# Optimization experiments

Hardware: AMD Instinct MI355X
Metric: run time of the kernel (lower is better)

Reference implementation:

```python
import jax, jax.numpy as jnp
import numpy as np

TAU = 0.5
EPS = 1e-12  # F.normalize eps


def _l2_normalize(z):
    n = jnp.linalg.norm(z, axis=1, keepdims=True)
    return z / jnp.maximum(n, EPS)


def _semi_loss(a, b):
    # a, b: [N, d], already raw embeddings; normalize then exp(sim/tau)
    an = _l2_normalize(a)
    bn = _l2_normalize(b)
    refl = jnp.exp(jnp.matmul(an, an.T) / TAU)      # [N, N]
    between = jnp.exp(jnp.matmul(an, bn.T) / TAU)   # [N, N]
    pos = jnp.diagonal(between)
    denom = refl.sum(axis=1) + between.sum(axis=1) - jnp.diagonal(refl)
    return -jnp.log(pos / denom)


def setup_inputs() -> dict:
    key = jax.random.key(0)
    k1, k2 = jax.random.split(key)
    z1 = jax.random.normal(k1, (8192, 256), dtype=jnp.float32)
    z2 = jax.random.normal(k2, (8192, 256), dtype=jnp.float32)
    return {"z1": z1, "z2": z2, "mean": 1}


def reference(z1, z2, mean):
    l1 = _semi_loss(z1, z2)
    l2 = _semi_loss(z2, z1)
    ret = (l1 + l2) * 0.5
    return ret.mean() if mean else ret.sum()
```

## Files before the change

kernel.cpp:

```cpp
#include <hip/hip_runtime.h>
#include <hip/hip_bf16.h>
#include <hip/hip_fp8.h>

#define N_ROWS 8192
#define NZ 16384
#define DIM 256
#define TAU_INV 2.0f
#define BT 128
#define AT 64
#define NTILE 128
#define NRI 256
#define NCHUNK 16
#define SEGT 4
#define NSEG 4224
#define PSTRIDE 1152

typedef float f32x4 __attribute__((ext_vector_type(4)));
typedef long lx2 __attribute__((ext_vector_type(2)));

__global__ __launch_bounds__(256) void normalize_kernel(
    const float* __restrict__ z1, const float* __restrict__ z2,
    unsigned char* __restrict__ Z8, float* __restrict__ pos)
{
    const int tid = threadIdx.x;
    const int wave = tid >> 6;
    const int lane = tid & 63;
    const int row = blockIdx.x * 4 + wave;

    const float4 a = ((const float4*)(z1 + (size_t)row * DIM))[lane];
    const float4 b = ((const float4*)(z2 + (size_t)row * DIM))[lane];

    auto wsum = [&](float v) -> float {
        #pragma unroll
        for (int m = 1; m < 64; m <<= 1) v += __shfl_xor(v, m, 64);
        return v;
    };

    const float na2 = wsum(a.x*a.x + a.y*a.y + a.z*a.z + a.w*a.w);
    const float nb2 = wsum(b.x*b.x + b.y*b.y + b.z*b.z + b.w*b.w);
    const float sa = 16.0f / sqrtf(na2);
    const float sb = 16.0f / sqrtf(nb2);

    const float av[4] = {a.x*sa, a.y*sa, a.z*sa, a.w*sa};
    const float bv[4] = {b.x*sb, b.y*sb, b.z*sb, b.w*sb};
    unsigned char pa[4], pb[4];
    float qd = 0.0f;
    #pragma unroll
    for (int k = 0; k < 4; ++k) {
        __hip_fp8_e4m3 qa(av[k]);
        __hip_fp8_e4m3 qb(bv[k]);
        pa[k] = qa.__x; pb[k] = qb.__x;
        qd += float(qa) * float(qb);
    }
    const int g  = (lane >> 1) & 7;
    const int pp = ((g & 3) << 1) | (g >> 2);
    const int off = (lane >> 4) * 64 + pp * 8 + (lane & 1) * 4;
    *(uchar4*)(Z8 + (size_t)row * DIM + off) = *(uchar4*)pa;
    *(uchar4*)(Z8 + (size_t)(N_ROWS + row) * DIM + off) = *(uchar4*)pb;

    qd = wsum(qd);
    if (lane == 0) pos[row] = qd * 0.00390625f;
}

template <bool TWO_STAGE>
__global__ __launch_bounds__(256, 3) void gram_kernel(
    const unsigned char* __restrict__ Z,
    float* __restrict__ part, float* __restrict__ S)
{
    const int sid = (blockIdx.x & 7) * (NSEG / 8) + (blockIdx.x >> 3);
    int g = (int)((260.0f - sqrtf(67600.0f - 16.0f * (float)sid)) * 0.125f);
    g = g < 0 ? 0 : (g > 31 ? 31 : g);
    while (260 * g - 4 * g * g > sid) --g;
    while (g < 31 && 260 * (g + 1) - 4 * (g + 1) * (g + 1) <= sid) ++g;
    const int local = sid - (260 * g - 4 * g * g);
    const int v  = 32 - g;
    const int r8i = local / v;
    const int s4 = local - r8i * v;
    const int ri = 8 * g + r8i;
    const int tj0 = (ri >> 1) + SEGT * s4;
    const int nt = (NTILE - tj0 < SEGT) ? (NTILE - tj0) : SEGT;

    __shared__ unsigned char Ls[49152];

    const int tid  = threadIdx.x;
    const int wave = tid >> 6;
    const int lane = tid & 63;
    const int wr = wave >> 1, wc = wave & 1;
    const int lm = lane & 15, lq = lane >> 4;

    const int r8 = lane >> 3;
    const int pg = lane & 7;
    const int G0 = pg ^ (r8 >> 1);
    const int dlt = 64 - ((G0 & 4) << 5);
    const unsigned char* pA =
        Z + (size_t)(ri * AT + wave * 16 + r8) * DIM + (G0 << 4);
    const unsigned char* pB0 =
        Z + (size_t)(tj0 * BT + wave * 32 + r8) * DIM + (G0 << 4);

    auto stageB = [&](const unsigned char* pb, int kh, int sl) {
        #pragma unroll
        for (int c = 0; c < 4; ++c) {
            const unsigned char* gb = ((c & 1) ? pb + dlt : pb) + c * 2048 + kh * 128;
            __builtin_amdgcn_global_load_lds(
                (const __attribute__((address_space(1))) void*)gb,
                (__attribute__((address_space(3))) void*)
                    (Ls + 16384 + sl * 16384 + (wave * 4 + c) * 1024), 16, 0, 0);
        }
    };

    #pragma unroll
    for (int kh = 0; kh < 2; ++kh)
        #pragma unroll
        for (int c = 0; c < 2; ++c) {
            const unsigned char* ga = ((c & 1) ? pA + dlt : pA) + c * 2048 + kh * 128;
            __builtin_amdgcn_global_load_lds(
                (const __attribute__((address_space(1))) void*)ga,
                (__attribute__((address_space(3))) void*)
                    (Ls + kh * 8192 + wave * 2048 + c * 1024), 16, 0, 0);
        }
    stageB(pB0, 0, 0);

    const int s0 = (lq ^ (lm >> 1)) << 4;
    const int s1 = s0 ^ 64;
    const unsigned char* LA = Ls + (wr * 32 + lm) * 128;
    const unsigned char* LB = Ls + 16384 + (wc * 64 + lm) * 128;

    const float SC = 2.8853900817779268f / 256.0f;

    f32x4 rowacc[2] = {};

    for (int t = 0; t < nt; ++t) {
        f32x4 acc[2][4] = {};
        #pragma unroll
        for (int kh = 0; kh < 2; ++kh) {
            __syncthreads();
            if (kh == 0)            stageB(pB0 + (size_t)t * 32768, 1, 1);
            else if (t + 1 < nt)    stageB(pB0 + (size_t)(t + 1) * 32768, 0, 0);

            const unsigned char* la = LA + (kh << 13);
            const unsigned char* lb = LB + (kh << 14);
            lx2 aP[2], bP[4];
            __builtin_amdgcn_s_setprio(1);
            #pragma unroll
            for (int f = 0; f < 2; ++f) aP[f] = *(const lx2*)(la + s0 + f * 2048);
            #pragma unroll
            for (int f = 0; f < 4; ++f) bP[f] = *(const lx2*)(lb + s0 + f * 2048);
            #pragma unroll
            for (int fr = 0; fr < 2; ++fr)
                #pragma unroll
                for (int fc = 0; fc < 4; ++fc) {
                    acc[fr][fc] = __builtin_amdgcn_mfma_f32_16x16x32_fp8_fp8(
                        aP[fr].x, bP[fc].x, acc[fr][fc], 0, 0, 0);
                    acc[fr][fc] = __builtin_amdgcn_mfma_f32_16x16x32_fp8_fp8(
                        aP[fr].y, bP[fc].y, acc[fr][fc], 0, 0, 0);
                }
            #pragma unroll
            for (int f = 0; f < 2; ++f) aP[f] = *(const lx2*)(la + s1 + f * 2048);
            #pragma unroll
            for (int f = 0; f < 4; ++f) bP[f] = *(const lx2*)(lb + s1 + f * 2048);
            #pragma unroll
            for (int fr = 0; fr < 2; ++fr)
                #pragma unroll
                for (int fc = 0; fc < 4; ++fc) {
                    acc[fr][fc] = __builtin_amdgcn_mfma_f32_16x16x32_fp8_fp8(
                        aP[fr].x, bP[fc].x, acc[fr][fc], 0, 0, 0);
                    acc[fr][fc] = __builtin_amdgcn_mfma_f32_16x16x32_fp8_fp8(
                        aP[fr].y, bP[fc].y, acc[fr][fc], 0, 0, 0);
                }
            __builtin_amdgcn_s_setprio(0);
        }

        #pragma unroll
        for (int fr = 0; fr < 2; ++fr)
            #pragma unroll
            for (int fc = 0; fc < 4; ++fc)
                #pragma unroll
                for (int r = 0; r < 4; ++r)
                    acc[fr][fc][r] = exp2f(acc[fr][fc][r] * SC);

        const int tj = tj0 + t;
        if (tj == (ri >> 1)) {
            const int add = (ri & 1) << 6;
            #pragma unroll
            for (int fr = 0; fr < 2; ++fr) {
                const int ciloc = wr * 32 + fr * 16 + lq * 4;
                #pragma unroll
                for (int fc = 0; fc < 4; ++fc) {
                    const int cj = wc * 64 + fc * 16 + lm;
                    #pragma unroll
                    for (int r = 0; r < 4; ++r)
                        if (cj <= ciloc + r + add) acc[fr][fc][r] = 0.0f;
                }
            }
        }

        #pragma unroll
        for (int fr = 0; fr < 2; ++fr)
            #pragma unroll
            for (int r = 0; r < 4; ++r)
                rowacc[fr][r] += acc[fr][0][r] + acc[fr][1][r]
                               + acc[fr][2][r] + acc[fr][3][r];

        float* dstc = TWO_STAGE ? (part + (size_t)sid * PSTRIDE + 128 + t * 256)
                                : nullptr;
        #pragma unroll
        for (int fc = 0; fc < 4; ++fc) {
            float s = 0.0f;
            #pragma unroll
            for (int fr = 0; fr < 2; ++fr)
                #pragma unroll
                for (int r = 0; r < 4; ++r) s += acc[fr][fc][r];
            s += __shfl_xor(s, 16, 64);
            s += __shfl_xor(s, 32, 64);
            if (lq == 0) {
                const int cc = wc * 64 + fc * 16 + lm;
                if (TWO_STAGE) dstc[wr * 128 + cc] = s;
                else atomicAdd(&S[tj * BT + cc], s);
            }
        }
    }

    float* dstr = TWO_STAGE ? (part + (size_t)sid * PSTRIDE) : nullptr;
    #pragma unroll
    for (int fr = 0; fr < 2; ++fr) {
        f32x4 rs;
        #pragma unroll
        for (int r = 0; r < 4; ++r) {
            float s = rowacc[fr][r];
            s += __shfl_xor(s, 1, 64);
            s += __shfl_xor(s, 2, 64);
            s += __shfl_xor(s, 4, 64);
            s += __shfl_xor(s, 8, 64);
            rs[r] = s;
        }
        if (lm == 0) {
            const int rr = wr * 32 + fr * 16 + lq * 4;
            if (TWO_STAGE) *(f32x4*)(dstr + wc * 64 + rr) = rs;
            else {
                #pragma unroll
                for (int r = 0; r < 4; ++r)
                    atomicAdd(&S[ri * AT + rr + r], rs[r]);
            }
        }
    }
}

__global__ __launch_bounds__(256) void reduce_kernel(
    const float* __restrict__ part, float* __restrict__ S2,
    float* __restrict__ out)
{
    const int chunk = blockIdx.y;
    const int tid = threadIdx.x;
    const int r = blockIdx.x * 256 + tid;
    const int ri = r >> 6, rr = r & 63;
    const int gg = ri >> 3;
    const int nseg = 32 - gg;
    const int sid0 = 260 * gg - 4 * gg * gg + (ri & 7) * nseg;
    const int tj = r >> 7, cc = r & 127;
    const int nr = 2 * tj + 2;
    const int T = 2 * nseg + 2 * nr;

    if (chunk == 0 && r == 0) out[0] = 0.0f;

    float s = 0.0f;
    for (int m = chunk; m < T; m += NCHUNK) {
        size_t addr;
        if (m < 2 * nseg) {
            const int sg = m >> 1;
            addr = (size_t)(sid0 + sg) * PSTRIDE + (m & 1) * 64 + rr;
        } else {
            const int m2 = m - 2 * nseg;
            const int rip = m2 >> 1;
            const int dtj = tj - (rip >> 1);
            const int gp = rip >> 3;
            const int sidc = 260 * gp - 4 * gp * gp + (rip & 7) * (32 - gp)
                           + (dtj >> 2);
            addr = (size_t)sidc * PSTRIDE + 128 + (dtj & 3) * 256
                 + (m2 & 1) * 128 + cc;
        }
        s += part[addr];
    }
    S2[(size_t)chunk * NZ + r] = s;
}

__global__ __launch_bounds__(256) void loss2_kernel(
    const float* __restrict__ S2, const float* __restrict__ pos,
    float* __restrict__ out)
{
    const int i = blockIdx.x * 256 + threadIdx.x;
    float den1 = 0.0f, den2 = 0.0f;
    #pragma unroll
    for (int c = 0; c < NCHUNK; ++c) {
        den1 += S2[(size_t)c * NZ + i];
        den2 += S2[(size_t)c * NZ + N_ROWS + i];
    }
    float v = 0.5f * (logf(den1) + logf(den2)) - TAU_INV * pos[i];

    __shared__ float red[4];
    #pragma unroll
    for (int m = 1; m < 64; m <<= 1) v += __shfl_xor(v, m, 64);
    if ((threadIdx.x & 63) == 0) red[threadIdx.x >> 6] = v;
    __syncthreads();
    if (threadIdx.x == 0)
        atomicAdd(out, (red[0] + red[1] + red[2] + red[3]) * (1.0f / N_ROWS));
}

__global__ __launch_bounds__(256) void loss_kernel(
    const float* __restrict__ S, const float* __restrict__ pos,
    float* __restrict__ out)
{
    const int i = blockIdx.x * 256 + threadIdx.x;
    float v = 0.5f * (logf(S[i]) + logf(S[N_ROWS + i])) - TAU_INV * pos[i];

    __shared__ float red[4];
    #pragma unroll
    for (int m = 1; m < 64; m <<= 1) v += __shfl_xor(v, m, 64);
    if ((threadIdx.x & 63) == 0) red[threadIdx.x >> 6] = v;
    __syncthreads();
    if (threadIdx.x == 0)
        atomicAdd(out, (red[0] + red[1] + red[2] + red[3]) * (1.0f / N_ROWS));
}

extern "C" void kernel_launch(void* const* d_in, const int* in_sizes, int n_in,
                              void* d_out, int out_size, void* d_ws, size_t ws_size,
                              hipStream_t stream)
{
    const float* z1 = (const float*)d_in[0];
    const float* z2 = (const float*)d_in[1];
    float* out = (float*)d_out;

    char* ws = (char*)d_ws;
    unsigned char* Z8 = (unsigned char*)ws;
    float* pos  = (float*)(ws + 4194304);
    float* S2   = (float*)(ws + 4227072);
    float* part = (float*)(ws + 5275648);
    const size_t need = 5275648 + (size_t)NSEG * PSTRIDE * 4;

    normalize_kernel<<<N_ROWS / 4, 256, 0, stream>>>(z1, z2, Z8, pos);

    if (ws_size >= need) {
        gram_kernel<true><<<NSEG, 256, 0, stream>>>(Z8, part, nullptr);
        dim3 rg(NZ / 256, NCHUNK);
        reduce_kernel<<<rg, 256, 0, stream>>>(part, S2, out);
        loss2_kernel<<<N_ROWS / 256, 256, 0, stream>>>(S2, pos, out);
    } else {
        hipMemsetAsync(S2, 0, NZ * sizeof(float), stream);
        hipMemsetAsync(out, 0, sizeof(float), stream);
        gram_kernel<false><<<NSEG, 256, 0, stream>>>(Z8, nullptr, S2);
        loss_kernel<<<N_ROWS / 256, 256, 0, stream>>>(S2, pos, out);
    }
}
```

Baseline: 157.5 us.

## Keep A fragments in registers and load B directly from global, dropping LDS staging

The gram kernel no longer stages A and B tiles through shared memory with global_load_lds and barriers. Each wave now holds the full 64-row A tile in registers and loads its own 32-column slice of B straight from global memory per k-half, which changes the wave decomposition from 2x2 to 1x4 along columns. The partial-sum layout shrinks because row partials are now per-wave (four 64-wide chunks) and column partials need one slot per tile, and the reduce kernel's indexing is updated to match. This removes LDS traffic and __syncthreads, but B reads now go uncoalesced through global/L2 with no prefetch overlap, and register pressure rises.

```diff
diff --git a/kernel.cpp b/kernel.cpp
--- a/kernel.cpp
+++ b/kernel.cpp
@@ -9,11 +9,10 @@
 #define BT 128
 #define AT 64
 #define NTILE 128
-#define NRI 256
 #define NCHUNK 16
 #define SEGT 4
 #define NSEG 4224
-#define PSTRIDE 1152
+#define PSTRIDE 768
 
 typedef float f32x4 __attribute__((ext_vector_type(4)));
 typedef long lx2 __attribute__((ext_vector_type(2)));
@@ -80,100 +79,59 @@
     const int tj0 = (ri >> 1) + SEGT * s4;
     const int nt = (NTILE - tj0 < SEGT) ? (NTILE - tj0) : SEGT;
 
-    __shared__ unsigned char Ls[49152];
-
     const int tid  = threadIdx.x;
-    const int wave = tid >> 6;
+    const int w    = tid >> 6;
     const int lane = tid & 63;
-    const int wr = wave >> 1, wc = wave & 1;
     const int lm = lane & 15, lq = lane >> 4;
 
-    const int r8 = lane >> 3;
-    const int pg = lane & 7;
-    const int G0 = pg ^ (r8 >> 1);
-    const int dlt = 64 - ((G0 & 4) << 5);
-    const unsigned char* pA =
-        Z + (size_t)(ri * AT + wave * 16 + r8) * DIM + (G0 << 4);
-    const unsigned char* pB0 =
-        Z + (size_t)(tj0 * BT + wave * 32 + r8) * DIM + (G0 << 4);
-
-    auto stageB = [&](const unsigned char* pb, int kh, int sl) {
-        #pragma unroll
-        for (int c = 0; c < 4; ++c) {
-            const unsigned char* gb = ((c & 1) ? pb + dlt : pb) + c * 2048 + kh * 128;
-            __builtin_amdgcn_global_load_lds(
-                (const __attribute__((address_space(1))) void*)gb,
-                (__attribute__((address_space(3))) void*)
-                    (Ls + 16384 + sl * 16384 + (wave * 4 + c) * 1024), 16, 0, 0);
-        }
-    };
-
-    #pragma unroll
-    for (int kh = 0; kh < 2; ++kh)
-        #pragma unroll
-        for (int c = 0; c < 2; ++c) {
-            const unsigned char* ga = ((c & 1) ? pA + dlt : pA) + c * 2048 + kh * 128;
-            __builtin_amdgcn_global_load_lds(
-                (const __attribute__((address_space(1))) void*)ga,
-                (__attribute__((address_space(3))) void*)
-                    (Ls + kh * 8192 + wave * 2048 + c * 1024), 16, 0, 0);
-        }
-    stageB(pB0, 0, 0);
-
-    const int s0 = (lq ^ (lm >> 1)) << 4;
-    const int s1 = s0 ^ 64;
-    const unsigned char* LA = Ls + (wr * 32 + lm) * 128;
-    const unsigned char* LB = Ls + 16384 + (wc * 64 + lm) * 128;
+    lx2 aR[2][2][4];
+    {
+        const unsigned char* pa = Z + (size_t)(ri * AT + lm) * DIM + lq * 16;
+        #pragma unroll
+        for (int fr = 0; fr < 4; ++fr)
+            #pragma unroll
+            for (int kh = 0; kh < 2; ++kh)
+                #pragma unroll
+                for (int s = 0; s < 2; ++s)
+                    aR[kh][s][fr] =
+                        *(const lx2*)(pa + fr * 4096 + kh * 128 + s * 64);
+    }
+
+    const unsigned char* pb =
+        Z + (size_t)(tj0 * BT + w * 32 + lm) * DIM + lq * 16;
 
     const float SC = 2.8853900817779268f / 256.0f;
 
-    f32x4 rowacc[2] = {};
+    f32x4 rowacc[4] = {};
 
     for (int t = 0; t < nt; ++t) {
-        f32x4 acc[2][4] = {};
+        f32x4 acc[4][2] = {};
         #pragma unroll
         for (int kh = 0; kh < 2; ++kh) {
-            __syncthreads();
-            if (kh == 0)            stageB(pB0 + (size_t)t * 32768, 1, 1);
-            else if (t + 1 < nt)    stageB(pB0 + (size_t)(t + 1) * 32768, 0, 0);
-
-            const unsigned char* la = LA + (kh << 13);
-            const unsigned char* lb = LB + (kh << 14);
-            lx2 aP[2], bP[4];
-            __builtin_amdgcn_s_setprio(1);
-            #pragma unroll
-            for (int f = 0; f < 2; ++f) aP[f] = *(const lx2*)(la + s0 + f * 2048);
-            #pragma unroll
-            for (int f = 0; f < 4; ++f) bP[f] = *(const lx2*)(lb + s0 + f * 2048);
-            #pragma unroll
-            for (int fr = 0; fr < 2; ++fr)
-                #pragma unroll
-                for (int fc = 0; fc < 4; ++fc) {
-                    acc[fr][fc] = __builtin_amdgcn_mfma_f32_16x16x32_fp8_fp8(
-                        aP[fr].x, bP[fc].x, acc[fr][fc], 0, 0, 0);
-                    acc[fr][fc] = __builtin_amdgcn_mfma_f32_16x16x32_fp8_fp8(
-                        aP[fr].y, bP[fc].y, acc[fr][fc], 0, 0, 0);
-                }
-            #pragma unroll
-            for (int f = 0; f < 2; ++f) aP[f] = *(const lx2*)(la + s1 + f * 2048);
-            #pragma unroll
-            for (int f = 0; f < 4; ++f) bP[f] = *(const lx2*)(lb + s1 + f * 2048);
-            #pragma unroll
-            for (int fr = 0; fr < 2; ++fr)
-                #pragma unroll
-                for (int fc = 0; fc < 4; ++fc) {
-                    acc[fr][fc] = __builtin_amdgcn_mfma_f32_16x16x32_fp8_fp8(
-                        aP[fr].x, bP[fc].x, acc[fr][fc], 0, 0, 0);
-                    acc[fr][fc] = __builtin_amdgcn_mfma_f32_16x16x32_fp8_fp8(
-                        aP[fr].y, bP[fc].y, acc[fr][fc], 0, 0, 0);
-                }
-            __builtin_amdgcn_s_setprio(0);
-        }
-
-        #pragma unroll
-        for (int fr = 0; fr < 2; ++fr)
-            #pragma unroll
-            for (int fc = 0; fc < 4; ++fc)
+            lx2 bP[2][2];
+            #pragma unroll
+            for (int fc = 0; fc < 2; ++fc)
+                #pragma unroll
+                for (int s = 0; s < 2; ++s)
+                    bP[s][fc] = *(const lx2*)
+                        (pb + (size_t)t * 32768 + fc * 4096 + kh * 128 + s * 64);
+            #pragma unroll
+            for (int s = 0; s < 2; ++s)
+                #pragma unroll
+                for (int fr = 0; fr < 4; ++fr)
+                    #pragma unroll
+                    for (int fc = 0; fc < 2; ++fc) {
+                        acc[fr][fc] = __builtin_amdgcn_mfma_f32_16x16x32_fp8_fp8(
+                            aR[kh][s][fr].x, bP[s][fc].x, acc[fr][fc], 0, 0, 0);
+                        acc[fr][fc] = __builtin_amdgcn_mfma_f32_16x16x32_fp8_fp8(
+                            aR[kh][s][fr].y, bP[s][fc].y, acc[fr][fc], 0, 0, 0);
+                    }
+        }
+
+        #pragma unroll
+        for (int fr = 0; fr < 4; ++fr)
+            #pragma unroll
+            for (int fc = 0; fc < 2; ++fc)
                 #pragma unroll
                 for (int r = 0; r < 4; ++r)
                     acc[fr][fc][r] = exp2f(acc[fr][fc][r] * SC);
@@ -182,47 +140,46 @@
         if (tj == (ri >> 1)) {
             const int add = (ri & 1) << 6;
             #pragma unroll
-            for (int fr = 0; fr < 2; ++fr) {
-                const int ciloc = wr * 32 + fr * 16 + lq * 4;
-                #pragma unroll
-                for (int fc = 0; fc < 4; ++fc) {
-                    const int cj = wc * 64 + fc * 16 + lm;
+            for (int fr = 0; fr < 4; ++fr) {
+                const int gi = fr * 16 + lq * 4;
+                #pragma unroll
+                for (int fc = 0; fc < 2; ++fc) {
+                    const int cj = w * 32 + fc * 16 + lm;
                     #pragma unroll
                     for (int r = 0; r < 4; ++r)
-                        if (cj <= ciloc + r + add) acc[fr][fc][r] = 0.0f;
+                        if (cj <= gi + r + add) acc[fr][fc][r] = 0.0f;
                 }
             }
         }
 
         #pragma unroll
-        for (int fr = 0; fr < 2; ++fr)
+        for (int fr = 0; fr < 4; ++fr)
             #pragma unroll
             for (int r = 0; r < 4; ++r)
-                rowacc[fr][r] += acc[fr][0][r] + acc[fr][1][r]
-                               + acc[fr][2][r] + acc[fr][3][r];
-
-        float* dstc = TWO_STAGE ? (part + (size_t)sid * PSTRIDE + 128 + t * 256)
+                rowacc[fr][r] += acc[fr][0][r] + acc[fr][1][r];
+
+        float* dstc = TWO_STAGE ? (part + (size_t)sid * PSTRIDE + 256 + t * 128)
                                 : nullptr;
         #pragma unroll
-        for (int fc = 0; fc < 4; ++fc) {
+        for (int fc = 0; fc < 2; ++fc) {
             float s = 0.0f;
             #pragma unroll
-            for (int fr = 0; fr < 2; ++fr)
+            for (int fr = 0; fr < 4; ++fr)
                 #pragma unroll
                 for (int r = 0; r < 4; ++r) s += acc[fr][fc][r];
             s += __shfl_xor(s, 16, 64);
             s += __shfl_xor(s, 32, 64);
             if (lq == 0) {
-                const int cc = wc * 64 + fc * 16 + lm;
-                if (TWO_STAGE) dstc[wr * 128 + cc] = s;
-                else atomicAdd(&S[tj * BT + cc], s);
+                const int cj = w * 32 + fc * 16 + lm;
+                if (TWO_STAGE) dstc[cj] = s;
+                else atomicAdd(&S[tj * BT + cj], s);
             }
         }
     }
 
     float* dstr = TWO_STAGE ? (part + (size_t)sid * PSTRIDE) : nullptr;
     #pragma unroll
-    for (int fr = 0; fr < 2; ++fr) {
+    for (int fr = 0; fr < 4; ++fr) {
         f32x4 rs;
         #pragma unroll
         for (int r = 0; r < 4; ++r) {
@@ -234,8 +191,8 @@
             rs[r] = s;
         }
         if (lm == 0) {
-            const int rr = wr * 32 + fr * 16 + lq * 4;
-            if (TWO_STAGE) *(f32x4*)(dstr + wc * 64 + rr) = rs;
+            const int rr = fr * 16 + lq * 4;
+            if (TWO_STAGE) *(f32x4*)(dstr + w * 64 + rr) = rs;
             else {
                 #pragma unroll
                 for (int r = 0; r < 4; ++r)
@@ -258,25 +215,22 @@
     const int sid0 = 260 * gg - 4 * gg * gg + (ri & 7) * nseg;
     const int tj = r >> 7, cc = r & 127;
     const int nr = 2 * tj + 2;
-    const int T = 2 * nseg + 2 * nr;
+    const int T = 4 * nseg + nr;
 
     if (chunk == 0 && r == 0) out[0] = 0.0f;
 
     float s = 0.0f;
     for (int m = chunk; m < T; m += NCHUNK) {
         size_t addr;
-        if (m < 2 * nseg) {
-            const int sg = m >> 1;
-            addr = (size_t)(sid0 + sg) * PSTRIDE + (m & 1) * 64 + rr;
+        if (m < 4 * nseg) {
+            addr = (size_t)(sid0 + (m >> 2)) * PSTRIDE + (m & 3) * 64 + rr;
         } else {
-            const int m2 = m - 2 * nseg;
-            const int rip = m2 >> 1;
+            const int rip = m - 4 * nseg;
             const int dtj = tj - (rip >> 1);
             const int gp = rip >> 3;
             const int sidc = 260 * gp - 4 * gp * gp + (rip & 7) * (32 - gp)
                            + (dtj >> 2);
-            addr = (size_t)sidc * PSTRIDE + 128 + (dtj & 3) * 256
-                 + (m2 & 1) * 128 + cc;
+            addr = (size_t)sidc * PSTRIDE + 256 + (dtj & 3) * 128 + cc;
         }
         s += part[addr];
     }
```

After: 186.1 us. +18.1%, slower.
